# Performance work log

Hardware: AMD Instinct MI355X
Metric: run time of the kernel (lower is better)

Reference implementation:

```python
import jax, jax.numpy as jnp
import numpy as np

D = 512      # hidden_size
H = 8        # num_heads
EPS = 1e-5   # torch LayerNorm default eps


def _ln(x, g, b):
    m = x.mean(-1, keepdims=True)
    v = ((x - m) ** 2).mean(-1, keepdims=True)
    return (x - m) * jax.lax.rsqrt(v + EPS) * g + b


def _xavier(k, shape):
    fan_in, fan_out = shape
    lim = (6.0 / (fan_in + fan_out)) ** 0.5
    return jax.random.uniform(k, shape, jnp.float32, -lim, lim)


def setup_inputs() -> dict:
    key = jax.random.key(0)
    ks = jax.random.split(key, 8)
    lengths = np.array([512, 640, 768, 896, 1024, 512, 768, 1024], dtype=np.int64)
    cum = np.concatenate([np.zeros(1, np.int64), np.cumsum(lengths)])  # [9], last = 6144
    T = int(cum[-1])
    return {
        "h_n": jax.random.normal(ks[0], (T, D), jnp.float32),
        "to_v_w": _xavier(ks[1], (D, D)), "to_v_b": jnp.zeros((D,), jnp.float32),
        "to_qk_w": _xavier(ks[2], (D, 2 * D)), "to_qk_b": jnp.zeros((2 * D,), jnp.float32),
        "proj_w": _xavier(ks[3], (D, D)), "proj_b": jnp.zeros((D,), jnp.float32),
        "ffn_w1": _xavier(ks[4], (D, 4 * D)), "ffn_b1": jnp.zeros((4 * D,), jnp.float32),
        "ffn_w2": _xavier(ks[5], (4 * D, D)), "ffn_b2": jnp.zeros((D,), jnp.float32),
        "ln1_g": jnp.ones((D,), jnp.float32), "ln1_b": jnp.zeros((D,), jnp.float32),
        "ln2_g": jnp.ones((D,), jnp.float32), "ln2_b": jnp.zeros((D,), jnp.float32),
        "num_query_cumsum": jnp.asarray(cum),
    }


def reference(h_n, to_v_w, to_v_b, to_qk_w, to_qk_b, proj_w, proj_b,
              ffn_w1, ffn_b1, ffn_w2, ffn_b2, ln1_g, ln1_b, ln2_g, ln2_b,
              num_query_cumsum):
    # --- static ragged layout (indices are constants) ---
    cum = np.asarray(num_query_cumsum)
    lengths = np.diff(cum)                       # [B]
    B = int(lengths.size)
    N = int(lengths.max())                       # max_num_nodes
    T = int(cum[-1])
    bid = np.repeat(np.arange(B), lengths)       # [T] graph id per token
    pos = np.arange(T) - cum[bid]                # [T] slot within graph
    pad_mask = np.arange(N)[None, :] >= lengths[:, None]  # [B, N], True = padding

    hd = D // H
    scale = hd ** -0.5

    # --- projections on the flat ragged tokens ---
    v = h_n @ to_v_w + to_v_b                    # [T, D]
    qk = h_n @ to_qk_w + to_qk_b                 # [T, 2D]
    q, k = qk[:, :D], qk[:, D:]

    # --- pad ragged -> dense [B, H, N, hd] ---
    def pad(x):
        xp = jnp.zeros((B, N, D), x.dtype).at[bid, pos].set(x)
        return xp.reshape(B, N, H, hd).transpose(0, 2, 1, 3)

    qp, kp, vp = pad(q), pad(k), pad(v)

    # --- dense masked softmax attention (keys masked at pad slots) ---
    scores = jnp.einsum('bhnd,bhmd->bhnm', qp, kp) * scale
    scores = jnp.where(pad_mask[:, None, None, :], -jnp.inf, scores)
    attn = jax.nn.softmax(scores, axis=-1)
    ctx = jnp.einsum('bhnm,bhmd->bhnd', attn, vp)

    # --- unpad back to flat [T, D] ---
    h_new = ctx.transpose(0, 2, 1, 3).reshape(B, N, D)[bid, pos]

    # --- residual + LN + FFN + LN (dropout = 0) ---
    h1 = _ln(h_n + (h_new @ proj_w + proj_b), ln1_g, ln1_b)
    ffn = jax.nn.gelu(h1 @ ffn_w1 + ffn_b1, approximate=False) @ ffn_w2 + ffn_b2
    return _ln(h1 + ffn, ln2_g, ln2_b)
```

## Files before the change

### kernel.cpp

```cpp
#include <hip/hip_runtime.h>

typedef __bf16 bf16;
typedef __bf16 bf16x8 __attribute__((ext_vector_type(8)));
typedef __bf16 bf16x4 __attribute__((ext_vector_type(4)));
typedef float  f32x4  __attribute__((ext_vector_type(4)));

#define MFMA16 __builtin_amdgcn_mfma_f32_16x16x32_bf16

__device__ __forceinline__ void gl2lds16(const bf16* g, bf16* l) {
  __builtin_amdgcn_global_load_lds(
      (const __attribute__((address_space(1))) unsigned int*)g,
      (__attribute__((address_space(3))) unsigned int*)l, 16, 0, 0);
}

__device__ __forceinline__ int dt_bf16(const void* g1) {
  return (((const unsigned*)g1)[0] == 0x3F800000u) ? 0 : 1;
}
__device__ __forceinline__ float load_any(const void* p, int i, int f) {
  return f ? (float)((const bf16*)p)[i] : ((const float*)p)[i];
}

__global__ __launch_bounds__(256) void prep_all(
    const void* __restrict__ h, const void* __restrict__ w_qk,
    const void* __restrict__ w_v, const void* __restrict__ w_pr,
    const void* __restrict__ w_f1, const void* __restrict__ w_f2,
    const void* __restrict__ b_qk, const void* __restrict__ b_v,
    const void* __restrict__ b_pr, const void* __restrict__ b_f1,
    const void* __restrict__ b_f2, const void* __restrict__ g1,
    const void* __restrict__ b1, const void* __restrict__ g2,
    const void* __restrict__ b2,
    bf16* __restrict__ hb, bf16* __restrict__ Wtqkv, bf16* __restrict__ Wtpr,
    bf16* __restrict__ Wtf1, bf16* __restrict__ Wtf2,
    float* __restrict__ vec, int T) {
  __shared__ bf16 tile[32][33];
  const int f = dt_bf16(g1);
  const int t = threadIdx.x;
  int b = blockIdx.x;
  const int HB = (T * 512) / 2048;

  if (b < HB) {
    const int i = (b * 256 + t) * 8;
    if (f) {
      *(bf16x8*)&hb[i] = *(const bf16x8*)((const bf16*)h + i);
    } else {
      const float* hf = (const float*)h;
      bf16x8 v;
#pragma unroll
      for (int j = 0; j < 8; j++) v[j] = (bf16)hf[i + j];
      *(bf16x8*)&hb[i] = v;
    }
    return;
  }
  b -= HB;

  if (b < 3072) {
    const void* in; bf16* out; int K, N;
    if (b < 512)       { in = w_qk; out = Wtqkv;                     K = 512;  N = 1024; }
    else if (b < 768)  { b -= 512;  in = w_v;  out = Wtqkv + (size_t)1024 * 512; K = 512; N = 512; }
    else if (b < 1024) { b -= 768;  in = w_pr; out = Wtpr;           K = 512;  N = 512; }
    else if (b < 2048) { b -= 1024; in = w_f1; out = Wtf1;           K = 512;  N = 2048; }
    else               { b -= 2048; in = w_f2; out = Wtf2;           K = 2048; N = 512; }
    const int tilesx = N / 32;
    const int bx = (b % tilesx) * 32, by = (b / tilesx) * 32;
    const int tx = t & 31, ty = t >> 5;
#pragma unroll
    for (int i = 0; i < 32; i += 8)
      tile[ty + i][tx] = (bf16)load_any(in, (by + ty + i) * N + bx + tx, f);
    __syncthreads();
#pragma unroll
    for (int i = 0; i < 32; i += 8)
      out[(size_t)(bx + ty + i) * K + by + tx] = tile[tx][ty + i];
    return;
  }
  b -= 3072;

  const int i = b * 256 + t;
  if (i >= 6656) return;
  const void* src; int base;
  if (i < 1024)      { src = b_qk; base = 0; }
  else if (i < 1536) { src = b_v;  base = 1024; }
  else if (i < 2048) { src = b_pr; base = 1536; }
  else if (i < 4096) { src = b_f1; base = 2048; }
  else if (i < 4608) { src = b_f2; base = 4096; }
  else if (i < 5120) { src = g1;   base = 4608; }
  else if (i < 5632) { src = b1;   base = 5120; }
  else if (i < 6144) { src = g2;   base = 5632; }
  else               { src = b2;   base = 6144; }
  vec[i] = load_any(src, i - base, f);
}

template <int BM, int MODE>
__global__ __launch_bounds__(256) void gemm_lds(const bf16* __restrict__ A,
                                                const bf16* __restrict__ Bt,
                                                const float* __restrict__ bias,
                                                void* __restrict__ aux,
                                                void* __restrict__ outp,
                                                void* __restrict__ outp2,
                                                int N, int K, int ldA, int ldB,
                                                int ldT) {
  constexpr int BN = 128;
  constexpr int WAVES_M = BM / 64;
  constexpr int WAVES_N = 4 / WAVES_M;
  constexpr int WN = BN / WAVES_N;
  constexpr int NI = WN / 16;
  __shared__ __align__(16) bf16 As[BM * 64];
  __shared__ __align__(16) bf16 Bs[BN * 64];
  const int t = threadIdx.x;
  const int m0 = blockIdx.x * BM, n0 = blockIdx.y * BN;
  const int lane = t & 63, wv = t >> 6;
  const int wm = (wv / WAVES_N) * 64;
  const int wn = (wv % WAVES_N) * WN;
  const int qd = lane >> 4, cl = lane & 15;
  const int koff = (MODE == 6) ? blockIdx.z * K : 0;

  const f32x4 fz = {0.f, 0.f, 0.f, 0.f};
  f32x4 acc[4][NI];
#pragma unroll
  for (int i = 0; i < 4; i++)
#pragma unroll
    for (int j = 0; j < NI; j++) acc[i][j] = fz;

  const int srow = wv * 8 + (lane >> 3);
  const int sch = (lane & 7) ^ (lane >> 3);
  const bf16* pA = A + (size_t)(m0 + srow) * ldA + koff + sch * 8;
  const bf16* pB = Bt + (size_t)(n0 + srow) * ldB + koff + sch * 8;
  bf16* AsW = As + wv * 8 * 64;
  bf16* BsW = Bs + wv * 8 * 64;

  for (int k0 = 0; k0 < K; k0 += 64) {
    __syncthreads();
#pragma unroll
    for (int op = 0; op < BM / 32; op++)
      gl2lds16(pA + (size_t)(op * 32) * ldA, AsW + op * 32 * 64);
#pragma unroll
    for (int op = 0; op < 4; op++)
      gl2lds16(pB + (size_t)(op * 32) * ldB, BsW + op * 32 * 64);
    pA += 64; pB += 64;
    __syncthreads();

#pragma unroll
    for (int ss = 0; ss < 2; ss++) {
      bf16x8 af[4], bfr[NI];
#pragma unroll
      for (int i = 0; i < 4; i++)
        af[i] = *(const bf16x8*)&As[(wm + i * 16 + cl) * 64 +
                                    ((ss * 4 + qd) ^ (cl & 7)) * 8];
#pragma unroll
      for (int i = 0; i < NI; i++)
        bfr[i] = *(const bf16x8*)&Bs[(wn + i * 16 + cl) * 64 +
                                     ((ss * 4 + qd) ^ (cl & 7)) * 8];
#pragma unroll
      for (int mi = 0; mi < 4; mi++)
#pragma unroll
        for (int ni = 0; ni < NI; ni++)
          acc[mi][ni] = MFMA16(af[mi], bfr[ni], acc[mi][ni], 0, 0, 0);
    }
  }

  float bv[NI];
#pragma unroll
  for (int ni = 0; ni < NI; ni++)
    bv[ni] = (MODE == 6) ? 0.f : bias[n0 + wn + ni * 16 + cl];

#pragma unroll
  for (int mi = 0; mi < 4; mi++) {
    const int mbase = m0 + wm + mi * 16 + qd * 4;
#pragma unroll
    for (int ni = 0; ni < NI; ni++) {
      const int n = n0 + wn + ni * 16 + cl;
      if (MODE == 5) {
        if (n0 < 1024) {
          bf16* out = (bf16*)outp;
#pragma unroll
          for (int r = 0; r < 4; r++)
            out[(size_t)(mbase + r) * 1024 + n] = (bf16)(acc[mi][ni][r] + bv[ni]);
        } else {
          bf16* vtp = (bf16*)aux;
          bf16x4 pk;
#pragma unroll
          for (int r = 0; r < 4; r++) pk[r] = (bf16)(acc[mi][ni][r] + bv[ni]);
          *(bf16x4*)&vtp[(size_t)(n - 1024) * ldT + mbase] = pk;
        }
      } else if (MODE == 2) {
        float* out = (float*)outp;
        const bf16* res = (const bf16*)aux;
#pragma unroll
        for (int r = 0; r < 4; r++)
          out[(size_t)(mbase + r) * N + n] =
              acc[mi][ni][r] + bv[ni] + (float)res[(size_t)(mbase + r) * N + n];
      } else if (MODE == 3) {
        bf16* out = (bf16*)outp;
#pragma unroll
        for (int r = 0; r < 4; r++) {
          float x = acc[mi][ni][r] + bv[ni];
          float gl = 0.5f * x * (1.0f + erff(x * 0.70710678118654752f));
          out[(size_t)(mbase + r) * N + n] = (bf16)gl;
        }
      } else {
        float* out = (float*)(blockIdx.z ? outp2 : outp);
#pragma unroll
        for (int r = 0; r < 4; r++)
          out[(size_t)(mbase + r) * N + n] = acc[mi][ni][r];
      }
    }
  }
}

__global__ __launch_bounds__(256) void attn_kernel(const bf16* __restrict__ qk,
                                                   const bf16* __restrict__ vt,
                                                   bf16* __restrict__ ctx,
                                                   const int* __restrict__ cumraw,
                                                   int T, int ncum) {
  __shared__ __align__(16) bf16 Ks[2][64 * 64];
  __shared__ __align__(16) bf16 Vs[2][64 * 64];
  __shared__ __align__(16) bf16 P[4][16 * 64];
  const int wv = threadIdx.x >> 6, lane = threadIdx.x & 63;
  const int qd = lane >> 4, cl = lane & 15;
  const int q0b = blockIdx.x * 64;
  const int q0 = q0b + wv * 16;
  const int h = blockIdx.y;

  const int stride = (cumraw[1] == 0) ? 2 : 1;
  int kstart = 0, kend = T;
  for (int i = 1; i < ncum; i++) {
    int c = cumraw[i * stride];
    if (c > q0b) { kend = c; break; }
    kstart = c;
  }

  const bf16* qbase = qk + (size_t)(q0 + cl) * 1024 + h * 64 + qd * 8;
  bf16x8 qf0 = *(const bf16x8*)qbase;
  bf16x8 qf1 = *(const bf16x8*)(qbase + 32);

  const f32x4 fz = {0.f, 0.f, 0.f, 0.f};
  f32x4 o[4] = {fz, fz, fz, fz};
  float lacc[4] = {0.f, 0.f, 0.f, 0.f};

  const int srow = wv * 8 + (lane >> 3);
  const int schunk = (lane & 7) ^ (srow & 7);
  const bf16* kg = qk + 512 + (size_t)h * 64 + schunk * 8;
  const bf16* vg = vt + (size_t)(h * 64 + srow) * T + schunk * 8;
  const int woff = wv * 8 * 64;

  const int bch = qd ^ (cl & 7);
  const float cc = 0.1803368801111204f;

  {
    const bf16* kg0 = kg + (size_t)(kstart + srow) * 1024;
    gl2lds16(kg0, Ks[0] + woff);
    gl2lds16(kg0 + (size_t)32 * 1024, Ks[0] + woff + 32 * 64);
    const bf16* vg0 = vg + kstart;
    gl2lds16(vg0, Vs[0] + woff);
    gl2lds16(vg0 + (size_t)32 * T, Vs[0] + woff + 32 * 64);
  }

  int ib = 0;
  for (int kc = kstart; kc < kend; kc += 64, ib ^= 1) {
    __syncthreads();

    if (kc + 64 < kend) {
      const bf16* kg0 = kg + (size_t)(kc + 64 + srow) * 1024;
      gl2lds16(kg0, Ks[ib ^ 1] + woff);
      gl2lds16(kg0 + (size_t)32 * 1024, Ks[ib ^ 1] + woff + 32 * 64);
      const bf16* vg0 = vg + kc + 64;
      gl2lds16(vg0, Vs[ib ^ 1] + woff);
      gl2lds16(vg0 + (size_t)32 * T, Vs[ib ^ 1] + woff + 32 * 64);
    }

    f32x4 s[4];
#pragma unroll
    for (int ni = 0; ni < 4; ni++) {
      const bf16* kr = Ks[ib] + (ni * 16 + cl) * 64;
      f32x4 tacc = fz;
      tacc = MFMA16(qf0, *(const bf16x8*)(kr + bch * 8), tacc, 0, 0, 0);
      tacc = MFMA16(qf1, *(const bf16x8*)(kr + (bch ^ 4) * 8), tacc, 0, 0, 0);
      s[ni] = tacc;
    }

    bf16* Pw = P[wv];
#pragma unroll
    for (int r = 0; r < 4; r++) {
      const float p0 = __builtin_amdgcn_exp2f(s[0][r] * cc);
      const float p1 = __builtin_amdgcn_exp2f(s[1][r] * cc);
      const float p2 = __builtin_amdgcn_exp2f(s[2][r] * cc);
      const float p3 = __builtin_amdgcn_exp2f(s[3][r] * cc);
      lacc[r] += (p0 + p1) + (p2 + p3);
      const int prow = qd * 4 + r;
      const int px = prow & 7;
      const int cb = cl >> 3, ci = cl & 7;
      Pw[prow * 64 + ((cb ^ px) * 8) + ci] = (bf16)p0;
      Pw[prow * 64 + (((2 + cb) ^ px) * 8) + ci] = (bf16)p1;
      Pw[prow * 64 + (((4 + cb) ^ px) * 8) + ci] = (bf16)p2;
      Pw[prow * 64 + (((6 + cb) ^ px) * 8) + ci] = (bf16)p3;
    }

    const int pch = qd ^ (cl & 7);
    const bf16* pr = Pw + cl * 64;
    bf16x8 pf0 = *(const bf16x8*)(pr + pch * 8);
    bf16x8 pf1 = *(const bf16x8*)(pr + (pch ^ 4) * 8);
#pragma unroll
    for (int dt = 0; dt < 4; dt++) {
      const bf16* vr = Vs[ib] + (dt * 16 + cl) * 64;
      o[dt] = MFMA16(pf0, *(const bf16x8*)(vr + bch * 8), o[dt], 0, 0, 0);
      o[dt] = MFMA16(pf1, *(const bf16x8*)(vr + (bch ^ 4) * 8), o[dt], 0, 0, 0);
    }
  }

  float linv[4];
#pragma unroll
  for (int r = 0; r < 4; r++) {
    float l = lacc[r];
    l += __shfl_xor(l, 1);
    l += __shfl_xor(l, 2);
    l += __shfl_xor(l, 4);
    l += __shfl_xor(l, 8);
    linv[r] = __builtin_amdgcn_rcpf(l);
  }
#pragma unroll
  for (int dt = 0; dt < 4; dt++) {
#pragma unroll
    for (int r = 0; r < 4; r++) {
      float y = o[dt][r] * linv[r];
      ctx[(size_t)(q0 + qd * 4 + r) * 512 + h * 64 + dt * 16 + cl] = (bf16)y;
    }
  }
}

__global__ __launch_bounds__(256) void ln_kernel(const float* __restrict__ s,
                                                 const float* __restrict__ g,
                                                 const float* __restrict__ b,
                                                 bf16* __restrict__ outb) {
  const int row = blockIdx.x * 4 + (threadIdx.x >> 6);
  const int lane = threadIdx.x & 63;
  const float4* sr = (const float4*)(s + (size_t)row * 512);
  float4 x0 = sr[lane];
  float4 x1 = sr[lane + 64];
  float sum = x0.x + x0.y + x0.z + x0.w + x1.x + x1.y + x1.z + x1.w;
  float sq = x0.x * x0.x + x0.y * x0.y + x0.z * x0.z + x0.w * x0.w +
             x1.x * x1.x + x1.y * x1.y + x1.z * x1.z + x1.w * x1.w;
#pragma unroll
  for (int off = 1; off < 64; off <<= 1) {
    sum += __shfl_xor(sum, off);
    sq += __shfl_xor(sq, off);
  }
  const float mean = sum * (1.0f / 512.0f);
  const float var = sq * (1.0f / 512.0f) - mean * mean;
  const float rs = rsqrtf(var + 1e-5f);
  const float4* gp = (const float4*)g;
  const float4* bp = (const float4*)b;
  float4 g0 = gp[lane], g1v = gp[lane + 64];
  float4 b0 = bp[lane], b1v = bp[lane + 64];
  float xv[8] = {x0.x, x0.y, x0.z, x0.w, x1.x, x1.y, x1.z, x1.w};
  float gv[8] = {g0.x, g0.y, g0.z, g0.w, g1v.x, g1v.y, g1v.z, g1v.w};
  float bb[8] = {b0.x, b0.y, b0.z, b0.w, b1v.x, b1v.y, b1v.z, b1v.w};
  bf16x4 o0, o1;
#pragma unroll
  for (int j = 0; j < 4; j++) {
    o0[j] = (bf16)((xv[j] - mean) * rs * gv[j] + bb[j]);
    o1[j] = (bf16)((xv[4 + j] - mean) * rs * gv[4 + j] + bb[4 + j]);
  }
  *(bf16x4*)&outb[(size_t)row * 512 + lane * 4] = o0;
  *(bf16x4*)&outb[(size_t)row * 512 + 256 + lane * 4] = o1;
}

__global__ __launch_bounds__(256) void ln2_kernel(const float* __restrict__ s2a,
                                                  const float* __restrict__ s2b,
                                                  const bf16* __restrict__ h1b,
                                                  const float* __restrict__ bias,
                                                  const float* __restrict__ g,
                                                  const float* __restrict__ b,
                                                  void* __restrict__ outb,
                                                  const void* __restrict__ g1probe) {
  const int row = blockIdx.x * 4 + (threadIdx.x >> 6);
  const int lane = threadIdx.x & 63;
  const float4* sa = (const float4*)(s2a + (size_t)row * 512);
  const float4* sb = (const float4*)(s2b + (size_t)row * 512);
  const float4* bi = (const float4*)bias;
  float4 a0 = sa[lane], a1 = sa[lane + 64];
  float4 c0 = sb[lane], c1 = sb[lane + 64];
  float4 v0 = bi[lane], v1 = bi[lane + 64];
  bf16x4 h0 = *(const bf16x4*)&h1b[(size_t)row * 512 + lane * 4];
  bf16x4 h1 = *(const bf16x4*)&h1b[(size_t)row * 512 + 256 + lane * 4];
  float x[8];
#pragma unroll
  for (int j = 0; j < 4; j++) {
    x[j] = (&a0.x)[j] + (&c0.x)[j] + (&v0.x)[j] + (float)h0[j];
    x[4 + j] = (&a1.x)[j] + (&c1.x)[j] + (&v1.x)[j] + (float)h1[j];
  }
  float sum = 0.f, sq = 0.f;
#pragma unroll
  for (int j = 0; j < 8; j++) { sum += x[j]; sq += x[j] * x[j]; }
#pragma unroll
  for (int off = 1; off < 64; off <<= 1) {
    sum += __shfl_xor(sum, off);
    sq += __shfl_xor(sq, off);
  }
  const float mean = sum * (1.0f / 512.0f);
  const float var = sq * (1.0f / 512.0f) - mean * mean;
  const float rs = rsqrtf(var + 1e-5f);
  const float4* gp = (const float4*)g;
  const float4* bp = (const float4*)b;
  float4 g0 = gp[lane], g1v = gp[lane + 64];
  float4 b0 = bp[lane], b1v = bp[lane + 64];
  float gv[8] = {g0.x, g0.y, g0.z, g0.w, g1v.x, g1v.y, g1v.z, g1v.w};
  float bb[8] = {b0.x, b0.y, b0.z, b0.w, b1v.x, b1v.y, b1v.z, b1v.w};
  float y[8];
#pragma unroll
  for (int j = 0; j < 8; j++) y[j] = (x[j] - mean) * rs * gv[j] + bb[j];

  if (dt_bf16(g1probe)) {
    bf16* ob = (bf16*)outb;
    bf16x4 o0, o1;
#pragma unroll
    for (int j = 0; j < 4; j++) { o0[j] = (bf16)y[j]; o1[j] = (bf16)y[4 + j]; }
    *(bf16x4*)&ob[(size_t)row * 512 + lane * 4] = o0;
    *(bf16x4*)&ob[(size_t)row * 512 + 256 + lane * 4] = o1;
  } else {
    float4* of = (float4*)((float*)outb + (size_t)row * 512);
    of[lane] = make_float4(y[0], y[1], y[2], y[3]);
    of[lane + 64] = make_float4(y[4], y[5], y[6], y[7]);
  }
}

extern "C" void kernel_launch(void* const* d_in, const int* in_sizes, int n_in,
                              void* d_out, int out_size, void* d_ws, size_t ws_size,
                              hipStream_t stream) {
  (void)n_in; (void)out_size; (void)ws_size;
  const void* h_n  = d_in[0];
  const void* w_v  = d_in[1];
  const void* b_v  = d_in[2];
  const void* w_qk = d_in[3];
  const void* b_qk = d_in[4];
  const void* w_pr = d_in[5];
  const void* b_pr = d_in[6];
  const void* w_f1 = d_in[7];
  const void* b_f1 = d_in[8];
  const void* w_f2 = d_in[9];
  const void* b_f2 = d_in[10];
  const void* g1w  = d_in[11];
  const void* b1w  = d_in[12];
  const void* g2w  = d_in[13];
  const void* b2w  = d_in[14];
  const int* cum   = (const int*)d_in[15];
  const int T = in_sizes[0] / 512;
  const int ncum = in_sizes[15];

  char* ws = (char*)d_ws;
  size_t off = 0;
  auto alloc = [&](size_t bytes) {
    char* p = ws + off;
    off += (bytes + 255) & ~(size_t)255;
    return p;
  };
  float* vec = (float*)alloc(6656 * 4);
  bf16* hb   = (bf16*)alloc((size_t)T * 512 * 2);
  bf16* qkb  = (bf16*)alloc((size_t)T * 1024 * 2);
  bf16* vt   = (bf16*)alloc((size_t)T * 512 * 2);
  bf16* ctx  = (bf16*)alloc((size_t)T * 512 * 2);
  float* s1  = (float*)alloc((size_t)T * 512 * 4);
  bf16* h1b  = (bf16*)alloc((size_t)T * 512 * 2);
  float* s2b = (float*)alloc((size_t)T * 512 * 4);
  bf16* Wtqkv = (bf16*)alloc((size_t)1536 * 512 * 2);
  bf16* Wtpr  = (bf16*)alloc((size_t)512 * 512 * 2);
  bf16* Wtf1  = (bf16*)alloc((size_t)2048 * 512 * 2);
  bf16* Wtf2  = (bf16*)alloc((size_t)512 * 2048 * 2);
  bf16* gbuf = qkb;
  float* s2a = s1;

  float* fb_qkv = vec + 0;
  float* fb_pr  = vec + 1536;
  float* fb_f1  = vec + 2048;
  float* fb_f2  = vec + 4096;
  float* fg1 = vec + 4608, *fb1 = vec + 5120;
  float* fg2 = vec + 5632, *fb2 = vec + 6144;

  const int prep_blocks = (T * 512) / 2048 + 3072 + 26;
  prep_all<<<prep_blocks, 256, 0, stream>>>(
      h_n, w_qk, w_v, w_pr, w_f1, w_f2,
      b_qk, b_v, b_pr, b_f1, b_f2, g1w, b1w, g2w, b2w,
      hb, Wtqkv, Wtpr, Wtf1, Wtf2, vec, T);

  gemm_lds<128, 5><<<dim3(T / 128, 12), 256, 0, stream>>>(
      hb, Wtqkv, fb_qkv, vt, qkb, nullptr, 1536, 512, 512, 512, T);
  attn_kernel<<<dim3(T / 64, 8), 256, 0, stream>>>(qkb, vt, ctx, cum, T, ncum);
  gemm_lds<64, 2><<<dim3(T / 64, 4), 256, 0, stream>>>(
      ctx, Wtpr, fb_pr, (void*)hb, s1, nullptr, 512, 512, 512, 512, 0);
  ln_kernel<<<T / 4, 256, 0, stream>>>(s1, fg1, fb1, h1b);
  gemm_lds<128, 3><<<dim3(T / 128, 16), 256, 0, stream>>>(
      h1b, Wtf1, fb_f1, nullptr, gbuf, nullptr, 2048, 512, 512, 512, 0);
  gemm_lds<128, 6><<<dim3(T / 128, 4, 2), 256, 0, stream>>>(
      gbuf, Wtf2, nullptr, nullptr, s2a, s2b, 512, 1024, 2048, 2048, 0);
  ln2_kernel<<<T / 4, 256, 0, stream>>>(s2a, s2b, h1b, fb_f2, fg2, fb2, d_out, g1w);
}
```

Measured before the change: 219.4 us.

## Replace erf GELU with tanh approximation and drop split-K in FFN2

The FFN1 epilogue now uses a tanh-form GELU built on hardware exp2/rcp instead of erff. The FFN2 GEMM loses its two-way split-K mode and becomes a single 64-row-tile GEMM whose epilogue adds bias and the h1 residual, so ln2 reads one fp32 buffer instead of two partial sums plus bias and residual. This cuts epilogue transcendental cost and the memory traffic of the extra partial buffer. The tradeoffs are fewer blocks per wave of FFN2 work, a longer K loop per block, and a GELU that differs from exact erf-based GELU by a small approximation error.

```diff
diff --git a/kernel.cpp b/kernel.cpp
--- a/kernel.cpp
+++ b/kernel.cpp
@@ -18,6 +18,12 @@
 }
 __device__ __forceinline__ float load_any(const void* p, int i, int f) {
   return f ? (float)((const bf16*)p)[i] : ((const float*)p)[i];
+}
+
+__device__ __forceinline__ float gelu_fast(float x) {
+  const float u = 0.7978845608028654f * (x + 0.044715f * x * x * x);
+  const float e = __builtin_amdgcn_exp2f(2.8853900817779268f * u);
+  return x * e * __builtin_amdgcn_rcpf(e + 1.0f);
 }
 
 __global__ __launch_bounds__(256) void prep_all(
@@ -95,7 +101,6 @@
                                                 const float* __restrict__ bias,
                                                 void* __restrict__ aux,
                                                 void* __restrict__ outp,
-                                                void* __restrict__ outp2,
                                                 int N, int K, int ldA, int ldB,
                                                 int ldT) {
   constexpr int BN = 128;
@@ -111,7 +116,6 @@
   const int wm = (wv / WAVES_N) * 64;
   const int wn = (wv % WAVES_N) * WN;
   const int qd = lane >> 4, cl = lane & 15;
-  const int koff = (MODE == 6) ? blockIdx.z * K : 0;
 
   const f32x4 fz = {0.f, 0.f, 0.f, 0.f};
   f32x4 acc[4][NI];
@@ -122,8 +126,8 @@
 
   const int srow = wv * 8 + (lane >> 3);
   const int sch = (lane & 7) ^ (lane >> 3);
-  const bf16* pA = A + (size_t)(m0 + srow) * ldA + koff + sch * 8;
-  const bf16* pB = Bt + (size_t)(n0 + srow) * ldB + koff + sch * 8;
+  const bf16* pA = A + (size_t)(m0 + srow) * ldA + sch * 8;
+  const bf16* pB = Bt + (size_t)(n0 + srow) * ldB + sch * 8;
   bf16* AsW = As + wv * 8 * 64;
   bf16* BsW = Bs + wv * 8 * 64;
 
@@ -159,8 +163,7 @@
 
   float bv[NI];
 #pragma unroll
-  for (int ni = 0; ni < NI; ni++)
-    bv[ni] = (MODE == 6) ? 0.f : bias[n0 + wn + ni * 16 + cl];
+  for (int ni = 0; ni < NI; ni++) bv[ni] = bias[n0 + wn + ni * 16 + cl];
 
 #pragma unroll
   for (int mi = 0; mi < 4; mi++) {
@@ -188,19 +191,11 @@
         for (int r = 0; r < 4; r++)
           out[(size_t)(mbase + r) * N + n] =
               acc[mi][ni][r] + bv[ni] + (float)res[(size_t)(mbase + r) * N + n];
-      } else if (MODE == 3) {
+      } else {
         bf16* out = (bf16*)outp;
 #pragma unroll
-        for (int r = 0; r < 4; r++) {
-          float x = acc[mi][ni][r] + bv[ni];
-          float gl = 0.5f * x * (1.0f + erff(x * 0.70710678118654752f));
-          out[(size_t)(mbase + r) * N + n] = (bf16)gl;
-        }
-      } else {
-        float* out = (float*)(blockIdx.z ? outp2 : outp);
-#pragma unroll
         for (int r = 0; r < 4; r++)
-          out[(size_t)(mbase + r) * N + n] = acc[mi][ni][r];
+          out[(size_t)(mbase + r) * N + n] = (bf16)gelu_fast(acc[mi][ni][r] + bv[ni]);
       }
     }
   }
@@ -363,33 +358,19 @@
   *(bf16x4*)&outb[(size_t)row * 512 + 256 + lane * 4] = o1;
 }
 
-__global__ __launch_bounds__(256) void ln2_kernel(const float* __restrict__ s2a,
-                                                  const float* __restrict__ s2b,
-                                                  const bf16* __restrict__ h1b,
-                                                  const float* __restrict__ bias,
+__global__ __launch_bounds__(256) void ln2_kernel(const float* __restrict__ s,
                                                   const float* __restrict__ g,
                                                   const float* __restrict__ b,
                                                   void* __restrict__ outb,
                                                   const void* __restrict__ g1probe) {
   const int row = blockIdx.x * 4 + (threadIdx.x >> 6);
   const int lane = threadIdx.x & 63;
-  const float4* sa = (const float4*)(s2a + (size_t)row * 512);
-  const float4* sb = (const float4*)(s2b + (size_t)row * 512);
-  const float4* bi = (const float4*)bias;
-  float4 a0 = sa[lane], a1 = sa[lane + 64];
-  float4 c0 = sb[lane], c1 = sb[lane + 64];
-  float4 v0 = bi[lane], v1 = bi[lane + 64];
-  bf16x4 h0 = *(const bf16x4*)&h1b[(size_t)row * 512 + lane * 4];
-  bf16x4 h1 = *(const bf16x4*)&h1b[(size_t)row * 512 + 256 + lane * 4];
-  float x[8];
-#pragma unroll
-  for (int j = 0; j < 4; j++) {
-    x[j] = (&a0.x)[j] + (&c0.x)[j] + (&v0.x)[j] + (float)h0[j];
-    x[4 + j] = (&a1.x)[j] + (&c1.x)[j] + (&v1.x)[j] + (float)h1[j];
-  }
-  float sum = 0.f, sq = 0.f;
-#pragma unroll
-  for (int j = 0; j < 8; j++) { sum += x[j]; sq += x[j] * x[j]; }
+  const float4* sr = (const float4*)(s + (size_t)row * 512);
+  float4 x0 = sr[lane];
+  float4 x1 = sr[lane + 64];
+  float sum = x0.x + x0.y + x0.z + x0.w + x1.x + x1.y + x1.z + x1.w;
+  float sq = x0.x * x0.x + x0.y * x0.y + x0.z * x0.z + x0.w * x0.w +
+             x1.x * x1.x + x1.y * x1.y + x1.z * x1.z + x1.w * x1.w;
 #pragma unroll
   for (int off = 1; off < 64; off <<= 1) {
     sum += __shfl_xor(sum, off);
@@ -402,11 +383,12 @@
   const float4* bp = (const float4*)b;
   float4 g0 = gp[lane], g1v = gp[lane + 64];
   float4 b0 = bp[lane], b1v = bp[lane + 64];
+  float xv[8] = {x0.x, x0.y, x0.z, x0.w, x1.x, x1.y, x1.z, x1.w};
   float gv[8] = {g0.x, g0.y, g0.z, g0.w, g1v.x, g1v.y, g1v.z, g1v.w};
   float bb[8] = {b0.x, b0.y, b0.z, b0.w, b1v.x, b1v.y, b1v.z, b1v.w};
   float y[8];
 #pragma unroll
-  for (int j = 0; j < 8; j++) y[j] = (x[j] - mean) * rs * gv[j] + bb[j];
+  for (int j = 0; j < 8; j++) y[j] = (xv[j] - mean) * rs * gv[j] + bb[j];
 
   if (dt_bf16(g1probe)) {
     bf16* ob = (bf16*)outb;
@@ -459,13 +441,12 @@
   bf16* ctx  = (bf16*)alloc((size_t)T * 512 * 2);
   float* s1  = (float*)alloc((size_t)T * 512 * 4);
   bf16* h1b  = (bf16*)alloc((size_t)T * 512 * 2);
-  float* s2b = (float*)alloc((size_t)T * 512 * 4);
   bf16* Wtqkv = (bf16*)alloc((size_t)1536 * 512 * 2);
   bf16* Wtpr  = (bf16*)alloc((size_t)512 * 512 * 2);
   bf16* Wtf1  = (bf16*)alloc((size_t)2048 * 512 * 2);
   bf16* Wtf2  = (bf16*)alloc((size_t)512 * 2048 * 2);
   bf16* gbuf = qkb;
-  float* s2a = s1;
+  float* s2 = s1;
 
   float* fb_qkv = vec + 0;
   float* fb_pr  = vec + 1536;
@@ -481,14 +462,14 @@
       hb, Wtqkv, Wtpr, Wtf1, Wtf2, vec, T);
 
   gemm_lds<128, 5><<<dim3(T / 128, 12), 256, 0, stream>>>(
-      hb, Wtqkv, fb_qkv, vt, qkb, nullptr, 1536, 512, 512, 512, T);
+      hb, Wtqkv, fb_qkv, vt, qkb, 1536, 512, 512, 512, T);
   attn_kernel<<<dim3(T / 64, 8), 256, 0, stream>>>(qkb, vt, ctx, cum, T, ncum);
   gemm_lds<64, 2><<<dim3(T / 64, 4), 256, 0, stream>>>(
-      ctx, Wtpr, fb_pr, (void*)hb, s1, nullptr, 512, 512, 512, 512, 0);
+      ctx, Wtpr, fb_pr, (void*)hb, s1, 512, 512, 512, 512, 0);
   ln_kernel<<<T / 4, 256, 0, stream>>>(s1, fg1, fb1, h1b);
   gemm_lds<128, 3><<<dim3(T / 128, 16), 256, 0, stream>>>(
-      h1b, Wtf1, fb_f1, nullptr, gbuf, nullptr, 2048, 512, 512, 512, 0);
-  gemm_lds<128, 6><<<dim3(T / 128, 4, 2), 256, 0, stream>>>(
-      gbuf, Wtf2, nullptr, nullptr, s2a, s2b, 512, 1024, 2048, 2048, 0);
-  ln2_kernel<<<T / 4, 256, 0, stream>>>(s2a, s2b, h1b, fb_f2, fg2, fb2, d_out, g1w);
-}
+      h1b, Wtf1, fb_f1, nullptr, gbuf, 2048, 512, 512, 512, 0);
+  gemm_lds<64, 2><<<dim3(T / 64, 4), 256, 0, stream>>>(
+      gbuf, Wtf2, fb_f2, (void*)h1b, s2, 512, 2048, 2048, 2048, 0);
+  ln2_kernel<<<T / 4, 256, 0, stream>>>(s2, fg2, fb2, d_out, g1w);
+}
```

Measured after the change: 219.2 us. No clear change (-0.1%).
